# Optimization experiments

Hardware: AMD Instinct MI355X
Metric: run time of the kernel (lower is better)

Reference implementation:

```python
import jax, jax.numpy as jnp
import numpy as np

D_MODEL = 1024
NUM_HEAD = 16
D_K = D_MODEL // NUM_HEAD
B, S = 2, 2048


def setup_inputs() -> dict:
    key = jax.random.key(0)
    ks = jax.random.split(key, 12)
    s = 1.0 / np.sqrt(D_MODEL)
    return {
        "x_q": jax.random.normal(ks[0], (B, S, D_MODEL), jnp.float32),
        "x_k": jax.random.normal(ks[1], (B, S, D_MODEL), jnp.float32),
        "x_v": jax.random.normal(ks[2], (B, S, D_MODEL), jnp.float32),
        "mask": jax.random.randint(ks[3], (B, S, S), 0, 2, jnp.int32),
        "Wq": jax.random.uniform(ks[4], (D_MODEL, D_MODEL), jnp.float32, -s, s),
        "bq": jax.random.uniform(ks[5], (D_MODEL,), jnp.float32, -s, s),
        "Wk": jax.random.uniform(ks[6], (D_MODEL, D_MODEL), jnp.float32, -s, s),
        "bk": jax.random.uniform(ks[7], (D_MODEL,), jnp.float32, -s, s),
        "Wv": jax.random.uniform(ks[8], (D_MODEL, D_MODEL), jnp.float32, -s, s),
        "bv": jax.random.uniform(ks[9], (D_MODEL,), jnp.float32, -s, s),
        "Wo": jax.random.uniform(ks[10], (D_MODEL, D_MODEL), jnp.float32, -s, s),
        "bo": jax.random.uniform(ks[11], (D_MODEL,), jnp.float32, -s, s),
    }


def reference(x_q, x_k, x_v, mask, Wq, bq, Wk, bk, Wv, bv, Wo, bo):
    # projections -> [B, H, S, d_k]
    def proj(x, W, b):
        y = x @ W.T + b
        return y.reshape(B, -1, NUM_HEAD, D_K).transpose(0, 2, 1, 3)

    q = proj(x_q, Wq, bq)
    k = proj(x_k, Wk, bk)
    v = proj(x_v, Wv, bv)
    scale = 1.0 / np.sqrt(D_K).astype(np.float32)
    scores = jnp.einsum("bhqd,bhkd->bhqk", q, k) * scale
    scores = jnp.where(mask[:, None, :, :] == 0, jnp.float32(-1e9), scores)
    p = jax.nn.softmax(scores, axis=-1)  # dropout is identity in eval mode
    attn = jnp.einsum("bhqk,bhkd->bhqd", p, v)
    concat = attn.transpose(0, 2, 1, 3).reshape(B, S, D_MODEL)
    return concat @ Wo.T + bo
```

## Files before the change

kernel.cpp:

```cpp
#include <hip/hip_runtime.h>
#include <cstdint>
#include <cstddef>

#define D_MODELX 1024
#define NUM_HEADX 16
#define D_KX 64
#define BBX 2
#define SSX 2048
#define M_TOK 4096
#define MBYTE (1u << 20)

typedef __attribute__((ext_vector_type(8))) short short8;
typedef __attribute__((ext_vector_type(4))) short short4v;
typedef __attribute__((ext_vector_type(4))) float float4v;
typedef __attribute__((ext_vector_type(2))) unsigned uint2v;
typedef __attribute__((ext_vector_type(4))) unsigned uint4v;

__device__ __forceinline__ short f2bf(float f) {
  unsigned u = __builtin_bit_cast(unsigned, f);
  u = u + 0x7FFFu + ((u >> 16) & 1u);
  return (short)(u >> 16);
}

__global__ void mask_bits_kernel(const int* __restrict__ mask, unsigned* __restrict__ mbits) {
  int i = blockIdx.x * blockDim.x + threadIdx.x;
  bool v = mask[i] != 0;
  unsigned long long bal = __ballot(v);
  int lane = threadIdx.x & 63;
  if (lane == 0)       mbits[i >> 5] = (unsigned)bal;
  else if (lane == 32) mbits[i >> 5] = (unsigned)(bal >> 32);
}

__global__ void cvt_w4_kernel(const float* __restrict__ w0, const float* __restrict__ w1,
                              const float* __restrict__ w2, const float* __restrict__ w3,
                              short* __restrict__ o0, short* __restrict__ o1,
                              short* __restrict__ o2, short* __restrict__ o3) {
  int z = blockIdx.y;
  const float* in = (z == 0) ? w0 : (z == 1) ? w1 : (z == 2) ? w2 : w3;
  short* out = (z == 0) ? o0 : (z == 1) ? o1 : (z == 2) ? o2 : o3;
  int i = blockIdx.x * blockDim.x + threadIdx.x;
  float4v v = ((const float4v*)in)[i];
  short4v s;
  s[0] = f2bf(v[0]); s[1] = f2bf(v[1]); s[2] = f2bf(v[2]); s[3] = f2bf(v[3]);
  ((short4v*)out)[i] = s;
}

__global__ void cvt_x3_kernel(const float* __restrict__ x0, const float* __restrict__ x1,
                              const float* __restrict__ x2,
                              short* __restrict__ o0, short* __restrict__ o1,
                              short* __restrict__ o2) {
  int z = blockIdx.y;
  const float* in = (z == 0) ? x0 : (z == 1) ? x1 : x2;
  short* out = (z == 0) ? o0 : (z == 1) ? o1 : o2;
  int i = blockIdx.x * blockDim.x + threadIdx.x;
  float4v v = ((const float4v*)in)[i];
  short4v s;
  s[0] = f2bf(v[0]); s[1] = f2bf(v[1]); s[2] = f2bf(v[2]); s[3] = f2bf(v[3]);
  ((short4v*)out)[i] = s;
}

#define GBK 64

__device__ __forceinline__ void gemm_body(const short* __restrict__ A,
                                          const short* __restrict__ Bw,
                                          const float* __restrict__ bias,
                                          float oscale, void* __restrict__ outp, int mode) {
  __shared__ short lds_a[128 * 64];
  __shared__ short lds_b[128 * 64];
  const int tid = threadIdx.x;
  const int lane = tid & 63;
  const int wid = tid >> 6;
  const int wm = wid >> 1, wn = wid & 1;
  const int bn = blockIdx.x, bm = blockIdx.y;
  const int l15 = lane & 15, lg = lane >> 4;

  const int s_row = tid >> 3;
  const int s_cB = ((tid & 7) << 4) ^ ((s_row & 7) << 4);
  const short* Abase = A + (size_t)(bm * 128) * 1024 + (s_cB >> 1);
  const short* Bbase = Bw + (size_t)(bn * 128) * 1024 + (s_cB >> 1);

  const int xmask = (l15 & 7) << 4;
  const int a_b0 = (wm * 64 + l15) * 128 + ((lg * 16) ^ xmask);
  const int a_b1 = (wm * 64 + l15) * 128 + ((64 + lg * 16) ^ xmask);
  const int b_b0 = (wn * 64 + l15) * 128 + ((lg * 16) ^ xmask);
  const int b_b1 = (wn * 64 + l15) * 128 + ((64 + lg * 16) ^ xmask);

  float4v acc[4][4];
#pragma unroll
  for (int m = 0; m < 4; ++m)
#pragma unroll
    for (int n = 0; n < 4; ++n) acc[m][n] = (float4v){0.f, 0.f, 0.f, 0.f};

  for (int kt = 0; kt < 1024; kt += GBK) {
#pragma unroll
    for (int it = 0; it < 4; ++it) {
      int row = it * 32 + s_row;
      __builtin_amdgcn_global_load_lds(
          (const uint32_t*)(Abase + (size_t)row * 1024 + kt),
          (uint32_t*)(lds_a + (it * 256 + wid * 64) * 8), 16, 0, 0);
      __builtin_amdgcn_global_load_lds(
          (const uint32_t*)(Bbase + (size_t)row * 1024 + kt),
          (uint32_t*)(lds_b + (it * 256 + wid * 64) * 8), 16, 0, 0);
    }
    __syncthreads();

    short8 af[4][2];
#pragma unroll
    for (int m = 0; m < 4; ++m) {
      af[m][0] = *(const short8*)((const char*)lds_a + a_b0 + m * 2048);
      af[m][1] = *(const short8*)((const char*)lds_a + a_b1 + m * 2048);
    }
#pragma unroll
    for (int n = 0; n < 4; ++n) {
      short8 b0 = *(const short8*)((const char*)lds_b + b_b0 + n * 2048);
      short8 b1 = *(const short8*)((const char*)lds_b + b_b1 + n * 2048);
#pragma unroll
      for (int m = 0; m < 4; ++m) {
        acc[m][n] = __builtin_amdgcn_mfma_f32_16x16x32_bf16(af[m][0], b0, acc[m][n], 0, 0, 0);
        acc[m][n] = __builtin_amdgcn_mfma_f32_16x16x32_bf16(af[m][1], b1, acc[m][n], 0, 0, 0);
      }
    }
    __syncthreads();
  }

#pragma unroll
  for (int n = 0; n < 4; ++n) {
    int col = bn * 128 + wn * 64 + n * 16 + l15;
    float bv = bias[col];
#pragma unroll
    for (int m = 0; m < 4; ++m) {
      if (mode == 2) {
        int base_row = bm * 128 + wm * 64 + m * 16 + lg * 4;
        int bidx = base_row >> 11, s = base_row & 2047;
        int h = col >> 6, d = col & 63;
        short4v sv;
#pragma unroll
        for (int r = 0; r < 4; ++r) sv[r] = f2bf(acc[m][n][r] + bv);
        *(short4v*)&((short*)outp)[(((size_t)(bidx * NUM_HEADX + h)) * D_KX + d) * SSX + s] = sv;
      } else {
#pragma unroll
        for (int r = 0; r < 4; ++r) {
          int row = bm * 128 + wm * 64 + m * 16 + lg * 4 + r;
          float val = (acc[m][n][r] + bv) * oscale;
          if (mode == 0) {
            int bidx = row >> 11, s = row & 2047;
            int h = col >> 6, d = col & 63;
            ((short*)outp)[(((size_t)(bidx * NUM_HEADX + h)) * SSX + s) * D_KX + d] = f2bf(val);
          } else {
            ((float*)outp)[(size_t)row * D_MODELX + col] = val;
          }
        }
      }
    }
  }
}

__global__ __launch_bounds__(256) void gemm_qkv_kernel(
    const short* __restrict__ xq, const short* __restrict__ xk, const short* __restrict__ xv,
    const short* __restrict__ wq, const short* __restrict__ wk, const short* __restrict__ wv,
    const float* __restrict__ bq, const float* __restrict__ bk, const float* __restrict__ bv,
    short* __restrict__ qo, short* __restrict__ ko, short* __restrict__ vo, float qs) {
  int z = blockIdx.z;
  const short* A = (z == 0) ? xq : (z == 1) ? xk : xv;
  const short* W = (z == 0) ? wq : (z == 1) ? wk : wv;
  const float* bi = (z == 0) ? bq : (z == 1) ? bk : bv;
  void* out = (z == 0) ? (void*)qo : (z == 1) ? (void*)ko : (void*)vo;
  float os = (z == 0) ? qs : 1.0f;
  int mode = (z == 2) ? 2 : 0;
  gemm_body(A, W, bi, os, out, mode);
}

__global__ __launch_bounds__(256) void gemm_one_kernel(const short* __restrict__ A,
                                                       const short* __restrict__ W,
                                                       const float* __restrict__ bias,
                                                       float os, void* __restrict__ out, int mode) {
  gemm_body(A, W, bias, os, out, mode);
}

__global__ __launch_bounds__(256, 3) void attn_kernel(const short* __restrict__ q_ws,
                                                      const short* __restrict__ k_ws,
                                                      const short* __restrict__ vT_ws,
                                                      const unsigned* __restrict__ mbits,
                                                      short* __restrict__ attn_ws,
                                                      short* __restrict__ opart,
                                                      float* __restrict__ lpart) {
  __shared__ short k_lds[2][4096];
  __shared__ short vT_lds[2][4096];
  __shared__ short p_lds[4][1024];

  const int tid = threadIdx.x;
  const int lane = tid & 63;
  const int w = tid >> 6;
  const int l15 = lane & 15, lg = lane >> 4;
  const int bid0 = blockIdx.x;
  const int bid = ((bid0 & 7) << 6) | (bid0 >> 3);
  const int qt = bid & 15;
  const int bh = bid >> 4;
  const int b = bh >> 4;
  const int h = bh & 15;
  const int z = blockIdx.z;
  const int nsplit = gridDim.z;
  const int nt = (SSX / 64) / nsplit;
  const int kb0 = z * nt * 64;

  const int qrow = qt * 128 + w * 32;

  const int xm15 = (l15 & 7) << 4;
  const int rd_c0 = l15 * 128 + ((lg * 16) ^ xm15);
  const int rd_c1 = l15 * 128 + ((64 + lg * 16) ^ xm15);
  char* kbase = (char*)k_lds;
  char* vbase = (char*)vT_lds;
  char* pwave = (char*)p_lds[w];
  const int s8 = ((l15 >> 2) & 3) << 3;
  const int pw_off = l15 * 32 + ((lg * 8) ^ s8);
  const int pr0 = (lg >> 1) * 512 + l15 * 32 + (((lg & 1) * 16) ^ s8);
  const int pr1 = pr0 ^ 8;

  const int srow = tid >> 2;
  const int scolS = (tid & 3) * 16;
  const int st0 = srow * 128 + ((scolS * 2) ^ ((srow & 7) << 4));
  const int st1 = srow * 128 + ((scolS * 2 + 16) ^ ((srow & 7) << 4));

  const short* kp = k_ws + (size_t)bh * SSX * D_KX + (size_t)srow * D_KX + scolS;
  const short* vp = vT_ws + (size_t)bh * D_KX * SSX + (size_t)srow * SSX + scolS;

  short8 qf[2][2];
#pragma unroll
  for (int qg = 0; qg < 2; ++qg)
#pragma unroll
    for (int c = 0; c < 2; ++c)
      qf[qg][c] = *(const short8*)(q_ws + ((size_t)bh * SSX + qrow + qg * 16 + l15) * D_KX + c * 32 + lg * 8);

  float4v acc[2][4];
#pragma unroll
  for (int qg = 0; qg < 2; ++qg)
#pragma unroll
    for (int db = 0; db < 4; ++db) acc[qg][db] = (float4v){0.f, 0.f, 0.f, 0.f};
  float l_part[2] = {0.f, 0.f};

  short8 kr0, kr1, vr0, vr1;
  auto loadt = [&](int kb) {
    const short* kq = kp + (size_t)kb * D_KX;
    kr0 = *(const short8*)kq;
    kr1 = *(const short8*)(kq + 8);
    const short* vq = vp + kb;
    vr0 = *(const short8*)vq;
    vr1 = *(const short8*)(vq + 8);
  };
  auto storet = [&](int BUF) {
    *(short8*)(kbase + BUF + st0) = kr0;
    *(short8*)(kbase + BUF + st1) = kr1;
    *(short8*)(vbase + BUF + st0) = vr0;
    *(short8*)(vbase + BUF + st1) = vr1;
  };

  const unsigned* mrow0 = mbits + ((size_t)b * SSX + qrow + l15) * (SSX / 32) + (kb0 >> 5);
  const unsigned* mrow1 = mbits + ((size_t)b * SSX + qrow + 16 + l15) * (SSX / 32) + (kb0 >> 5);
  unsigned long long mw0 = *(const unsigned long long*)mrow0, mwn0 = 0;
  unsigned long long mw1 = *(const unsigned long long*)mrow1, mwn1 = 0;

  loadt(kb0);
  storet(0);
  loadt(kb0 + 64);
  __syncthreads();

  auto step = [&](int t, int CURB, int NXTB) {
    float p[2][4][4];
    __builtin_amdgcn_s_setprio(1);
#pragma unroll
    for (int kf = 0; kf < 4; ++kf) {
      short8 k0 = *(const short8*)(kbase + CURB + rd_c0 + kf * 2048);
      short8 k1 = *(const short8*)(kbase + CURB + rd_c1 + kf * 2048);
      float4v f0 = (float4v){0.f, 0.f, 0.f, 0.f};
      f0 = __builtin_amdgcn_mfma_f32_16x16x32_bf16(k0, qf[0][0], f0, 0, 0, 0);
      f0 = __builtin_amdgcn_mfma_f32_16x16x32_bf16(k1, qf[0][1], f0, 0, 0, 0);
      float4v f1 = (float4v){0.f, 0.f, 0.f, 0.f};
      f1 = __builtin_amdgcn_mfma_f32_16x16x32_bf16(k0, qf[1][0], f1, 0, 0, 0);
      f1 = __builtin_amdgcn_mfma_f32_16x16x32_bf16(k1, qf[1][1], f1, 0, 0, 0);
#pragma unroll
      for (int r = 0; r < 4; ++r) { p[0][kf][r] = f0[r]; p[1][kf][r] = f1[r]; }
    }
    __builtin_amdgcn_s_setprio(0);

    if (t < nt - 1) storet(NXTB);
    if (t < nt - 2) loadt(kb0 + (t + 2) * 64);
    if (t < nt - 1) {
      mwn0 = *(const unsigned long long*)(mrow0 + 2 * (t + 1));
      mwn1 = *(const unsigned long long*)(mrow1 + 2 * (t + 1));
    }

#pragma unroll
    for (int qg = 0; qg < 2; ++qg) {
      unsigned long long sh = (qg == 0 ? mw0 : mw1) >> (lg * 4);
      unsigned mlo = (unsigned)sh, mhi = (unsigned)(sh >> 32);
      float tsum = 0.f;
#pragma unroll
      for (int kf = 0; kf < 4; ++kf) {
        float pv_[4];
#pragma unroll
        for (int r = 0; r < 4; ++r) {
          float pv = __builtin_amdgcn_exp2f(p[qg][kf][r]);
          unsigned bit = (kf < 2 ? mlo : mhi) & (1u << ((kf & 1) * 16 + r));
          pv_[r] = bit ? pv : 0.0f;
        }
        tsum += (pv_[0] + pv_[1]) + (pv_[2] + pv_[3]);
        unsigned u0, u1;
        asm("v_cvt_pk_bf16_f32 %0, %1, %2" : "=v"(u0) : "v"(pv_[0]), "v"(pv_[1]));
        asm("v_cvt_pk_bf16_f32 %0, %1, %2" : "=v"(u1) : "v"(pv_[2]), "v"(pv_[3]));
        *(uint2v*)(pwave + pw_off + kf * 512) = (uint2v){u0, u1};
      }
      l_part[qg] += tsum;

      short8 pa0, pa1;
      {
        uint2v a0 = *(const uint2v*)(pwave + pr0);
        uint2v a1 = *(const uint2v*)(pwave + pr1);
        pa0 = __builtin_bit_cast(short8, (uint4v){a0[0], a0[1], a1[0], a1[1]});
        uint2v b0 = *(const uint2v*)(pwave + pr0 + 1024);
        uint2v b1 = *(const uint2v*)(pwave + pr1 + 1024);
        pa1 = __builtin_bit_cast(short8, (uint4v){b0[0], b0[1], b1[0], b1[1]});
      }

      __builtin_amdgcn_s_setprio(1);
#pragma unroll
      for (int db = 0; db < 4; ++db) {
        short8 vb0 = *(const short8*)(vbase + CURB + rd_c0 + db * 2048);
        short8 vb1 = *(const short8*)(vbase + CURB + rd_c1 + db * 2048);
        acc[qg][db] = __builtin_amdgcn_mfma_f32_16x16x32_bf16(vb0, pa0, acc[qg][db], 0, 0, 0);
        acc[qg][db] = __builtin_amdgcn_mfma_f32_16x16x32_bf16(vb1, pa1, acc[qg][db], 0, 0, 0);
      }
      __builtin_amdgcn_s_setprio(0);
    }

    __syncthreads();
    mw0 = mwn0;
    mw1 = mwn1;
  };

  for (int t2 = 0; t2 < nt / 2; ++t2) {
    step(2 * t2, 0, 8192);
    step(2 * t2 + 1, 8192, 0);
  }

#pragma unroll
  for (int qg = 0; qg < 2; ++qg) {
    float lp = l_part[qg];
    lp += __shfl_xor(lp, 16);
    lp += __shfl_xor(lp, 32);
    const int q = qrow + qg * 16 + l15;
    if (nsplit == 1) {
      float inv = 1.0f / lp;
      size_t ttok = (size_t)b * SSX + q;
#pragma unroll
      for (int db = 0; db < 4; ++db) {
        short4v sv;
#pragma unroll
        for (int r = 0; r < 4; ++r) sv[r] = f2bf(acc[qg][db][r] * inv);
        *(short4v*)&attn_ws[ttok * D_MODELX + h * 64 + db * 16 + lg * 4] = sv;
      }
    } else {
      size_t rowp = ((size_t)z * 32 + bh) * SSX + q;
      if (lg == 0) lpart[rowp] = lp;
#pragma unroll
      for (int db = 0; db < 4; ++db) {
        short4v sv;
#pragma unroll
        for (int r = 0; r < 4; ++r) sv[r] = f2bf(acc[qg][db][r]);
        *(short4v*)&opart[rowp * D_KX + db * 16 + lg * 4] = sv;
      }
    }
  }
}

__global__ void combine_kernel(const short* __restrict__ opart, const float* __restrict__ lpart,
                               short* __restrict__ attn_ws) {
  int gtid = blockIdx.x * blockDim.x + threadIdx.x;
  int row = gtid >> 3;
  int dc = (gtid & 7) * 8;
  int bh = row >> 11, s = row & 2047;
  int b = bh >> 4, h = bh & 15;
  float inv = 1.0f / (lpart[row] + lpart[row + 32 * SSX]);
  short8 o0 = *(const short8*)&opart[(size_t)row * D_KX + dc];
  short8 o1 = *(const short8*)&opart[((size_t)row + 32 * SSX) * D_KX + dc];
  short8 sv;
#pragma unroll
  for (int j = 0; j < 8; ++j) {
    float f0 = __builtin_bit_cast(float, ((unsigned)(unsigned short)o0[j]) << 16);
    float f1 = __builtin_bit_cast(float, ((unsigned)(unsigned short)o1[j]) << 16);
    sv[j] = f2bf((f0 + f1) * inv);
  }
  *(short8*)&attn_ws[(((size_t)b * SSX + s) * D_MODELX) + h * 64 + dc] = sv;
}

extern "C" void kernel_launch(void* const* d_in, const int* in_sizes, int n_in,
                              void* d_out, int out_size, void* d_ws, size_t ws_size,
                              hipStream_t stream) {
  const float* x_q = (const float*)d_in[0];
  const float* x_k = (const float*)d_in[1];
  const float* x_v = (const float*)d_in[2];
  const int*   mask = (const int*)d_in[3];
  const float* Wq = (const float*)d_in[4];
  const float* bq = (const float*)d_in[5];
  const float* Wk = (const float*)d_in[6];
  const float* bk = (const float*)d_in[7];
  const float* Wv = (const float*)d_in[8];
  const float* bv = (const float*)d_in[9];
  const float* Wo = (const float*)d_in[10];
  const float* bo = (const float*)d_in[11];

  const float QSCALE = 0.125f * 1.44269504089f;

  char* ws = (char*)d_ws;
  short* q_ws  = (short*)(ws + 0 * MBYTE);
  short* k_ws  = (short*)(ws + 8 * MBYTE);
  short* vT_ws = (short*)(ws + 16 * MBYTE);

  dim3 ggrid(D_MODELX / 128, M_TOK / 128);

  if (ws_size >= (size_t)56 * MBYTE) {
    short* wq_bf = (short*)(ws + 24 * MBYTE);
    short* wk_bf = (short*)(ws + 26 * MBYTE);
    short* wv_bf = (short*)(ws + 28 * MBYTE);
    short* wo_bf = (short*)(ws + 30 * MBYTE);
    short* xq_bf = (short*)(ws + 32 * MBYTE);
    short* xk_bf = (short*)(ws + 40 * MBYTE);
    short* xv_bf = (short*)(ws + 48 * MBYTE);
    unsigned* mbits = (unsigned*)(ws + 24 * MBYTE);
    float* lpart    = (float*)(ws + 25 * MBYTE);
    short* attn_ws  = (short*)(ws + 32 * MBYTE);
    short* opart    = (short*)(ws + 40 * MBYTE);

    cvt_w4_kernel<<<dim3(1024, 4), 256, 0, stream>>>(Wq, Wk, Wv, Wo, wq_bf, wk_bf, wv_bf, wo_bf);
    cvt_x3_kernel<<<dim3(4096, 3), 256, 0, stream>>>(x_q, x_k, x_v, xq_bf, xk_bf, xv_bf);

    dim3 qkvgrid(D_MODELX / 128, M_TOK / 128, 3);
    gemm_qkv_kernel<<<qkvgrid, 256, 0, stream>>>(xq_bf, xk_bf, xv_bf, wq_bf, wk_bf, wv_bf,
                                                 bq, bk, bv, q_ws, k_ws, vT_ws, QSCALE);

    mask_bits_kernel<<<(BBX * SSX * SSX) / 256, 256, 0, stream>>>(mask, mbits);

    dim3 agrid(BBX * NUM_HEADX * (SSX / 128), 1, 2);
    attn_kernel<<<agrid, 256, 0, stream>>>(q_ws, k_ws, vT_ws, mbits, attn_ws, opart, lpart);
    combine_kernel<<<2048, 256, 0, stream>>>(opart, lpart, attn_ws);

    gemm_one_kernel<<<ggrid, 256, 0, stream>>>(attn_ws, wo_bf, bo, 1.0f, d_out, 1);
  } else {
    unsigned* mbits = (unsigned*)(ws + 24 * MBYTE);
    short* w_bf = (short*)(ws + 25 * MBYTE);
    short* x_bf = (short*)(ws + 27 * MBYTE);
    short* attn_ws = (short*)(ws + 27 * MBYTE);

    mask_bits_kernel<<<(BBX * SSX * SSX) / 256, 256, 0, stream>>>(mask, mbits);

    cvt_w4_kernel<<<dim3(1024, 1), 256, 0, stream>>>(Wq, Wq, Wq, Wq, w_bf, w_bf, w_bf, w_bf);
    cvt_x3_kernel<<<dim3(4096, 1), 256, 0, stream>>>(x_q, x_q, x_q, x_bf, x_bf, x_bf);
    gemm_one_kernel<<<ggrid, 256, 0, stream>>>(x_bf, w_bf, bq, QSCALE, q_ws, 0);

    cvt_w4_kernel<<<dim3(1024, 1), 256, 0, stream>>>(Wk, Wk, Wk, Wk, w_bf, w_bf, w_bf, w_bf);
    cvt_x3_kernel<<<dim3(4096, 1), 256, 0, stream>>>(x_k, x_k, x_k, x_bf, x_bf, x_bf);
    gemm_one_kernel<<<ggrid, 256, 0, stream>>>(x_bf, w_bf, bk, 1.0f, k_ws, 0);

    cvt_w4_kernel<<<dim3(1024, 1), 256, 0, stream>>>(Wv, Wv, Wv, Wv, w_bf, w_bf, w_bf, w_bf);
    cvt_x3_kernel<<<dim3(4096, 1), 256, 0, stream>>>(x_v, x_v, x_v, x_bf, x_bf, x_bf);
    gemm_one_kernel<<<ggrid, 256, 0, stream>>>(x_bf, w_bf, bv, 1.0f, vT_ws, 2);

    dim3 agrid(BBX * NUM_HEADX * (SSX / 128), 1, 1);
    attn_kernel<<<agrid, 256, 0, stream>>>(q_ws, k_ws, vT_ws, mbits, attn_ws, nullptr, nullptr);

    cvt_w4_kernel<<<dim3(1024, 1), 256, 0, stream>>>(Wo, Wo, Wo, Wo, w_bf, w_bf, w_bf, w_bf);
    gemm_one_kernel<<<ggrid, 256, 0, stream>>>(attn_ws, w_bf, bo, 1.0f, d_out, 1);
  }
}
```

Baseline: 167.2 us.

## Switch attention to 32x32x16 MFMA with permlane32 swap instead of LDS P staging

The attention inner loop now uses 32x32x16 bf16 MFMA tiles, so each wave computes a full 32-query by 32-key score block. The probability matrix is converted into the B-operand layout in registers with v_permlane32_swap rather than a round trip through a per-wave LDS buffer. This removes the p_lds shared memory and its write/read traffic and lowers the MFMA instruction count. In exchange, 16-wide accumulators raise register pressure, so the launch bounds occupancy hint drops from 3 to 2 blocks per CU.

```diff
diff --git a/kernel.cpp b/kernel.cpp
--- a/kernel.cpp
+++ b/kernel.cpp
@@ -13,6 +13,7 @@
 typedef __attribute__((ext_vector_type(8))) short short8;
 typedef __attribute__((ext_vector_type(4))) short short4v;
 typedef __attribute__((ext_vector_type(4))) float float4v;
+typedef __attribute__((ext_vector_type(16))) float float16v;
 typedef __attribute__((ext_vector_type(2))) unsigned uint2v;
 typedef __attribute__((ext_vector_type(4))) unsigned uint4v;
 
@@ -177,7 +178,7 @@
   gemm_body(A, W, bias, os, out, mode);
 }
 
-__global__ __launch_bounds__(256, 3) void attn_kernel(const short* __restrict__ q_ws,
+__global__ __launch_bounds__(256, 2) void attn_kernel(const short* __restrict__ q_ws,
                                                       const short* __restrict__ k_ws,
                                                       const short* __restrict__ vT_ws,
                                                       const unsigned* __restrict__ mbits,
@@ -186,12 +187,11 @@
                                                       float* __restrict__ lpart) {
   __shared__ short k_lds[2][4096];
   __shared__ short vT_lds[2][4096];
-  __shared__ short p_lds[4][1024];
 
   const int tid = threadIdx.x;
   const int lane = tid & 63;
   const int w = tid >> 6;
-  const int l15 = lane & 15, lg = lane >> 4;
+  const int l31 = lane & 31, hi = lane >> 5;
   const int bid0 = blockIdx.x;
   const int bid = ((bid0 & 7) << 6) | (bid0 >> 3);
   const int qt = bid & 15;
@@ -204,17 +204,14 @@
   const int kb0 = z * nt * 64;
 
   const int qrow = qt * 128 + w * 32;
-
-  const int xm15 = (l15 & 7) << 4;
-  const int rd_c0 = l15 * 128 + ((lg * 16) ^ xm15);
-  const int rd_c1 = l15 * 128 + ((64 + lg * 16) ^ xm15);
+  const int q = qrow + l31;
+
+  const int xm = (lane & 7) << 4;
+  int rd[4];
+#pragma unroll
+  for (int j = 0; j < 4; ++j) rd[j] = l31 * 128 + ((j * 32 + hi * 16) ^ xm);
   char* kbase = (char*)k_lds;
   char* vbase = (char*)vT_lds;
-  char* pwave = (char*)p_lds[w];
-  const int s8 = ((l15 >> 2) & 3) << 3;
-  const int pw_off = l15 * 32 + ((lg * 8) ^ s8);
-  const int pr0 = (lg >> 1) * 512 + l15 * 32 + (((lg & 1) * 16) ^ s8);
-  const int pr1 = pr0 ^ 8;
 
   const int srow = tid >> 2;
   const int scolS = (tid & 3) * 16;
@@ -224,19 +221,17 @@
   const short* kp = k_ws + (size_t)bh * SSX * D_KX + (size_t)srow * D_KX + scolS;
   const short* vp = vT_ws + (size_t)bh * D_KX * SSX + (size_t)srow * SSX + scolS;
 
-  short8 qf[2][2];
-#pragma unroll
-  for (int qg = 0; qg < 2; ++qg)
-#pragma unroll
-    for (int c = 0; c < 2; ++c)
-      qf[qg][c] = *(const short8*)(q_ws + ((size_t)bh * SSX + qrow + qg * 16 + l15) * D_KX + c * 32 + lg * 8);
-
-  float4v acc[2][4];
-#pragma unroll
-  for (int qg = 0; qg < 2; ++qg)
-#pragma unroll
-    for (int db = 0; db < 4; ++db) acc[qg][db] = (float4v){0.f, 0.f, 0.f, 0.f};
-  float l_part[2] = {0.f, 0.f};
+  short8 qf[4];
+#pragma unroll
+  for (int ds = 0; ds < 4; ++ds)
+    qf[ds] = *(const short8*)(q_ws + ((size_t)bh * SSX + q) * D_KX + ds * 16 + hi * 8);
+
+  float16v acc[2];
+#pragma unroll
+  for (int db = 0; db < 2; ++db)
+#pragma unroll
+    for (int i = 0; i < 16; ++i) acc[db][i] = 0.f;
+  float l_own = 0.f;
 
   short8 kr0, kr1, vr0, vr1;
   auto loadt = [&](int kb) {
@@ -254,10 +249,8 @@
     *(short8*)(vbase + BUF + st1) = vr1;
   };
 
-  const unsigned* mrow0 = mbits + ((size_t)b * SSX + qrow + l15) * (SSX / 32) + (kb0 >> 5);
-  const unsigned* mrow1 = mbits + ((size_t)b * SSX + qrow + 16 + l15) * (SSX / 32) + (kb0 >> 5);
-  unsigned long long mw0 = *(const unsigned long long*)mrow0, mwn0 = 0;
-  unsigned long long mw1 = *(const unsigned long long*)mrow1, mwn1 = 0;
+  const unsigned* mrow = mbits + ((size_t)b * SSX + q) * (SSX / 32) + (kb0 >> 5);
+  unsigned long long mw = *(const unsigned long long*)mrow, mwn = 0;
 
   loadt(kb0);
   storet(0);
@@ -265,76 +258,78 @@
   __syncthreads();
 
   auto step = [&](int t, int CURB, int NXTB) {
-    float p[2][4][4];
-    __builtin_amdgcn_s_setprio(1);
-#pragma unroll
-    for (int kf = 0; kf < 4; ++kf) {
-      short8 k0 = *(const short8*)(kbase + CURB + rd_c0 + kf * 2048);
-      short8 k1 = *(const short8*)(kbase + CURB + rd_c1 + kf * 2048);
-      float4v f0 = (float4v){0.f, 0.f, 0.f, 0.f};
-      f0 = __builtin_amdgcn_mfma_f32_16x16x32_bf16(k0, qf[0][0], f0, 0, 0, 0);
-      f0 = __builtin_amdgcn_mfma_f32_16x16x32_bf16(k1, qf[0][1], f0, 0, 0, 0);
-      float4v f1 = (float4v){0.f, 0.f, 0.f, 0.f};
-      f1 = __builtin_amdgcn_mfma_f32_16x16x32_bf16(k0, qf[1][0], f1, 0, 0, 0);
-      f1 = __builtin_amdgcn_mfma_f32_16x16x32_bf16(k1, qf[1][1], f1, 0, 0, 0);
-#pragma unroll
-      for (int r = 0; r < 4; ++r) { p[0][kf][r] = f0[r]; p[1][kf][r] = f1[r]; }
-    }
-    __builtin_amdgcn_s_setprio(0);
-
-    if (t < nt - 1) storet(NXTB);
-    if (t < nt - 2) loadt(kb0 + (t + 2) * 64);
-    if (t < nt - 1) {
-      mwn0 = *(const unsigned long long*)(mrow0 + 2 * (t + 1));
-      mwn1 = *(const unsigned long long*)(mrow1 + 2 * (t + 1));
-    }
-
-#pragma unroll
-    for (int qg = 0; qg < 2; ++qg) {
-      unsigned long long sh = (qg == 0 ? mw0 : mw1) >> (lg * 4);
-      unsigned mlo = (unsigned)sh, mhi = (unsigned)(sh >> 32);
-      float tsum = 0.f;
-#pragma unroll
-      for (int kf = 0; kf < 4; ++kf) {
+    unsigned long long shv = mw >> (hi * 4);
+
+    auto do_kb = [&](const float16v& s, int kb, int CURB_) {
+      unsigned wvm = (kb == 0) ? (unsigned)shv : (unsigned)(shv >> 32);
+      unsigned cw[8];
+      float ls = 0.f;
+#pragma unroll
+      for (int qd = 0; qd < 4; ++qd) {
         float pv_[4];
 #pragma unroll
         for (int r = 0; r < 4; ++r) {
-          float pv = __builtin_amdgcn_exp2f(p[qg][kf][r]);
-          unsigned bit = (kf < 2 ? mlo : mhi) & (1u << ((kf & 1) * 16 + r));
-          pv_[r] = bit ? pv : 0.0f;
+          float e = __builtin_amdgcn_exp2f(s[qd * 4 + r]);
+          e = ((wvm >> (qd * 8 + r)) & 1u) ? e : 0.f;
+          ls += e;
+          pv_[r] = e;
         }
-        tsum += (pv_[0] + pv_[1]) + (pv_[2] + pv_[3]);
         unsigned u0, u1;
         asm("v_cvt_pk_bf16_f32 %0, %1, %2" : "=v"(u0) : "v"(pv_[0]), "v"(pv_[1]));
         asm("v_cvt_pk_bf16_f32 %0, %1, %2" : "=v"(u1) : "v"(pv_[2]), "v"(pv_[3]));
-        *(uint2v*)(pwave + pw_off + kf * 512) = (uint2v){u0, u1};
-      }
-      l_part[qg] += tsum;
-
-      short8 pa0, pa1;
-      {
-        uint2v a0 = *(const uint2v*)(pwave + pr0);
-        uint2v a1 = *(const uint2v*)(pwave + pr1);
-        pa0 = __builtin_bit_cast(short8, (uint4v){a0[0], a0[1], a1[0], a1[1]});
-        uint2v b0 = *(const uint2v*)(pwave + pr0 + 1024);
-        uint2v b1 = *(const uint2v*)(pwave + pr1 + 1024);
-        pa1 = __builtin_bit_cast(short8, (uint4v){b0[0], b0[1], b1[0], b1[1]});
-      }
-
-      __builtin_amdgcn_s_setprio(1);
-#pragma unroll
-      for (int db = 0; db < 4; ++db) {
-        short8 vb0 = *(const short8*)(vbase + CURB + rd_c0 + db * 2048);
-        short8 vb1 = *(const short8*)(vbase + CURB + rd_c1 + db * 2048);
-        acc[qg][db] = __builtin_amdgcn_mfma_f32_16x16x32_bf16(vb0, pa0, acc[qg][db], 0, 0, 0);
-        acc[qg][db] = __builtin_amdgcn_mfma_f32_16x16x32_bf16(vb1, pa1, acc[qg][db], 0, 0, 0);
-      }
-      __builtin_amdgcn_s_setprio(0);
-    }
+        cw[qd * 2] = u0;
+        cw[qd * 2 + 1] = u1;
+      }
+      l_own += ls;
+#pragma unroll
+      for (int g = 0; g < 2; ++g) {
+        unsigned a0 = cw[2 * g * 2],     b0 = cw[(2 * g + 1) * 2];
+        unsigned a1 = cw[2 * g * 2 + 1], b1 = cw[(2 * g + 1) * 2 + 1];
+        asm("v_permlane32_swap_b32 %0, %1" : "+v"(a0), "+v"(b0));
+        asm("v_permlane32_swap_b32 %0, %1" : "+v"(a1), "+v"(b1));
+        short8 Bf = __builtin_bit_cast(short8, (uint4v){a0, a1, b0, b1});
+        __builtin_amdgcn_s_setprio(1);
+#pragma unroll
+        for (int db = 0; db < 2; ++db) {
+          short8 vf = *(const short8*)(vbase + CURB_ + db * 4096 + rd[kb * 2 + g]);
+          acc[db] = __builtin_amdgcn_mfma_f32_32x32x16_bf16(vf, Bf, acc[db], 0, 0, 0);
+        }
+        __builtin_amdgcn_s_setprio(0);
+      }
+    };
+
+    float16v s0;
+#pragma unroll
+    for (int i = 0; i < 16; ++i) s0[i] = 0.f;
+    __builtin_amdgcn_s_setprio(1);
+#pragma unroll
+    for (int ds = 0; ds < 4; ++ds) {
+      short8 kf_ = *(const short8*)(kbase + CURB + rd[ds]);
+      s0 = __builtin_amdgcn_mfma_f32_32x32x16_bf16(kf_, qf[ds], s0, 0, 0, 0);
+    }
+    __builtin_amdgcn_s_setprio(0);
+
+    if (t < nt - 1) storet(NXTB);
+    if (t < nt - 2) loadt(kb0 + (t + 2) * 64);
+    if (t < nt - 1) mwn = *(const unsigned long long*)(mrow + 2 * (t + 1));
+
+    do_kb(s0, 0, CURB);
+
+    float16v s1;
+#pragma unroll
+    for (int i = 0; i < 16; ++i) s1[i] = 0.f;
+    __builtin_amdgcn_s_setprio(1);
+#pragma unroll
+    for (int ds = 0; ds < 4; ++ds) {
+      short8 kf_ = *(const short8*)(kbase + CURB + 4096 + rd[ds]);
+      s1 = __builtin_amdgcn_mfma_f32_32x32x16_bf16(kf_, qf[ds], s1, 0, 0, 0);
+    }
+    __builtin_amdgcn_s_setprio(0);
+
+    do_kb(s1, 1, CURB);
 
     __syncthreads();
-    mw0 = mwn0;
-    mw1 = mwn1;
+    mw = mwn;
   };
 
   for (int t2 = 0; t2 < nt / 2; ++t2) {
@@ -342,33 +337,31 @@
     step(2 * t2 + 1, 8192, 0);
   }
 
-#pragma unroll
-  for (int qg = 0; qg < 2; ++qg) {
-    float lp = l_part[qg];
-    lp += __shfl_xor(lp, 16);
-    lp += __shfl_xor(lp, 32);
-    const int q = qrow + qg * 16 + l15;
-    if (nsplit == 1) {
-      float inv = 1.0f / lp;
-      size_t ttok = (size_t)b * SSX + q;
-#pragma unroll
-      for (int db = 0; db < 4; ++db) {
+  float lp = l_own + __shfl_xor(l_own, 32);
+  if (nsplit == 1) {
+    float inv = 1.0f / lp;
+    size_t ttok = (size_t)b * SSX + q;
+#pragma unroll
+    for (int db = 0; db < 2; ++db)
+#pragma unroll
+      for (int qd = 0; qd < 4; ++qd) {
         short4v sv;
 #pragma unroll
-        for (int r = 0; r < 4; ++r) sv[r] = f2bf(acc[qg][db][r] * inv);
-        *(short4v*)&attn_ws[ttok * D_MODELX + h * 64 + db * 16 + lg * 4] = sv;
-      }
-    } else {
-      size_t rowp = ((size_t)z * 32 + bh) * SSX + q;
-      if (lg == 0) lpart[rowp] = lp;
-#pragma unroll
-      for (int db = 0; db < 4; ++db) {
+        for (int r = 0; r < 4; ++r) sv[r] = f2bf(acc[db][qd * 4 + r] * inv);
+        *(short4v*)&attn_ws[ttok * D_MODELX + h * 64 + db * 32 + qd * 8 + hi * 4] = sv;
+      }
+  } else {
+    size_t rowp = ((size_t)z * 32 + bh) * SSX + q;
+    if (hi == 0) lpart[rowp] = lp;
+#pragma unroll
+    for (int db = 0; db < 2; ++db)
+#pragma unroll
+      for (int qd = 0; qd < 4; ++qd) {
         short4v sv;
 #pragma unroll
-        for (int r = 0; r < 4; ++r) sv[r] = f2bf(acc[qg][db][r]);
-        *(short4v*)&opart[rowp * D_KX + db * 16 + lg * 4] = sv;
-      }
-    }
+        for (int r = 0; r < 4; ++r) sv[r] = f2bf(acc[db][qd * 4 + r]);
+        *(short4v*)&opart[rowp * D_KX + db * 32 + qd * 8 + hi * 4] = sv;
+      }
   }
 }
 
```

New measurement: 163.3 us. -2.4%, faster.
